# Kernel optimization log

Hardware: AMD Instinct MI355X
Metric: run time of the kernel (lower is better)

## Reference

```python
import jax, jax.numpy as jnp
import numpy as np

ATOM_DIM = 128; RBF_DIM = 32; GEOM_HID = 128; SCAT = 64; OUT = 64; CUTOFF = 5.0
MAX_Z = 100; Z_EMB = 32; E_DIM = 32; PAIR_HID = 64
B = 16; N = 64; P = 8000; NE = 80


def _lin(key, i, o):
    kw, kb = jax.random.split(key)
    W = jax.random.normal(kw, (i, o), jnp.float32) / np.sqrt(i).astype(np.float32)
    b = jax.random.normal(kb, (o,), jnp.float32) * 0.01
    return W, b


def setup_inputs() -> dict:
    key = jax.random.key(0)
    ks = jax.random.split(key, 24)
    inp = {}
    inp["h_flat"] = jax.random.normal(ks[0], (B * N, ATOM_DIM), jnp.float32)
    inp["z_flat"] = jax.random.randint(ks[1], (B * N,), 0, MAX_Z + 1)
    inp["e_feat"] = jax.random.normal(ks[2], (NE, E_DIM), jnp.float32)
    inp["path_j"] = jax.random.randint(ks[3], (P,), 0, B * N)
    inp["path_k"] = jax.random.randint(ks[4], (P,), 0, B * N)
    # distances in (0, 1.2*cutoff) so some paths exceed the cutoff
    inp["path_r0j"] = jax.random.uniform(ks[5], (P,), jnp.float32, 0.1, 1.2 * CUTOFF)
    inp["path_r0k"] = jax.random.uniform(ks[6], (P,), jnp.float32, 0.1, 1.2 * CUTOFF)
    inp["path_rjk"] = jax.random.uniform(ks[7], (P,), jnp.float32, 0.1, 1.2 * CUTOFF)
    inp["path_cosangle"] = jax.random.uniform(ks[8], (P,), jnp.float32, -1.0, 1.0)
    inp["path_batch"] = jnp.sort(jax.random.randint(ks[9], (P,), 0, B))
    inp["bsz"] = B
    # params
    inp["z_emb"] = jax.random.normal(ks[10], (MAX_Z + 1, Z_EMB), jnp.float32)
    pe_in = 2 * Z_EMB + E_DIM
    inp["pe_w1"], inp["pe_b1"] = _lin(ks[11], pe_in, PAIR_HID)
    inp["pe_w2"], inp["pe_b2"] = _lin(ks[12], PAIR_HID, PAIR_HID)
    inp["pe_w3"], inp["pe_b3"] = _lin(ks[13], PAIR_HID, SCAT)
    gm_in = 2 * ATOM_DIM + 3 * RBF_DIM + 1
    inp["gm_w1"], inp["gm_b1"] = _lin(ks[14], gm_in, GEOM_HID)
    inp["gm_w2"], inp["gm_b2"] = _lin(ks[15], GEOM_HID, GEOM_HID)
    inp["gm_w3"], inp["gm_b3"] = _lin(ks[16], GEOM_HID, SCAT)
    inp["op_w1"], inp["op_b1"] = _lin(ks[17], SCAT, GEOM_HID)
    inp["op_w2"], inp["op_b2"] = _lin(ks[18], GEOM_HID, OUT)
    return inp


def _rbf(r):
    centers = jnp.linspace(0.0, CUTOFF, RBF_DIM)
    width = centers[1] - centers[0]
    return jnp.exp(-0.5 * ((r[..., None] - centers) / width) ** 2)


def _cutoff_fn(r):
    return 0.5 * (jnp.cos(jnp.pi * r / CUTOFF) + 1.0) * (r < CUTOFF)


def _mlp3(x, w1, b1, w2, b2, w3, b3):
    h = jax.nn.silu(x @ w1 + b1)
    h = jax.nn.silu(h @ w2 + b2)
    return h @ w3 + b3


def _mlp2(x, w1, b1, w2, b2):
    return jax.nn.silu(x @ w1 + b1) @ w2 + b2


def reference(h_flat, z_flat, e_feat, path_j, path_k, path_r0j, path_r0k,
              path_rjk, path_cosangle, path_batch, bsz, z_emb,
              pe_w1, pe_b1, pe_w2, pe_b2, pe_w3, pe_b3,
              gm_w1, gm_b1, gm_w2, gm_b2, gm_w3, gm_b3,
              op_w1, op_b1, op_w2, op_b2):
    n_e = e_feat.shape[0]
    n_p = path_j.shape[0]
    # gather atom features
    hj = h_flat[path_j]                                  # (P, atom_dim)
    hk = h_flat[path_k]
    f0j = _rbf(jnp.minimum(path_r0j, CUTOFF))            # (P, rbf_dim)
    f0k = _rbf(jnp.minimum(path_r0k, CUTOFF))
    fjk = _rbf(jnp.minimum(path_rjk, CUTOFF))
    geom_in = jnp.concatenate([hj, hk, f0j, f0k, fjk, path_cosangle[:, None]], axis=-1)
    g_geom = _mlp3(geom_in, gm_w1, gm_b1, gm_w2, gm_b2, gm_w3, gm_b3)  # (P, scat)
    # element-pair energy features
    ej = z_emb[z_flat[path_j]]                           # (P, z_emb)
    ek = z_emb[z_flat[path_k]]
    pair_in = jnp.concatenate([
        jnp.broadcast_to(ej[:, None, :], (n_p, n_e, ej.shape[-1])),
        jnp.broadcast_to(ek[:, None, :], (n_p, n_e, ek.shape[-1])),
        jnp.broadcast_to(e_feat[None, :, :], (n_p, n_e, e_feat.shape[-1])),
    ], axis=-1)                                          # (P, nE, 2*z_emb+e_dim)
    g_elem = _mlp3(pair_in, pe_w1, pe_b1, pe_w2, pe_b2, pe_w3, pe_b3)  # (P, nE, scat)
    # cutoff weights and outer-product contribution
    cw = _cutoff_fn(path_r0j) * _cutoff_fn(path_r0k) * _cutoff_fn(path_rjk)  # (P,)
    contrib = g_geom[:, None, :] * g_elem * cw[:, None, None]          # (P, nE, scat)
    # scatter-add into batch bins
    agg = jax.ops.segment_sum(contrib, path_batch, num_segments=bsz)   # (B, nE, scat)
    norm = jax.ops.segment_sum(cw, path_batch, num_segments=bsz)       # (B,)
    agg = agg / jnp.maximum(norm, 1e-8)[:, None, None]
    return _mlp2(agg, op_w1, op_b1, op_w2, op_b2)                      # (B, nE, out)
```

## Files before the change

kernel.cpp:

```cpp
#include <hip/hip_runtime.h>
#include <math.h>

typedef float f32x4 __attribute__((ext_vector_type(4)));
typedef short bf16x8 __attribute__((ext_vector_type(8)));
typedef unsigned short u16;

#define RBF_DIM 32
#define CUTOFF 5.0f
#define PI_F 3.14159265358979323846f
#define BB 16
#define PP 8000
#define NEE 80

#define CW_OFF      0
#define GCW_OFF     8000
#define AGG_OFF     520000
#define ZEJW_OFF    601920
#define ZEKW_OFF    608384
#define EFWB_OFF    614848
#define NORM_OFF    619968
#define AIDX_OFF    619984
#define ZJA_OFF     627984
#define ZKA_OFF     635984
#define BOFF_OFF    643984
#define BCNT_OFF    644004
#define BSUM_OFF    644036
#define BCNTB_OFF   644548
#define BLKOFF_OFF  645060
#define CHS_OFF     645096
#define CHC_OFF     645362
#define CHB_OFF     645628
#define NC_OFF      645894
#define W2THI_OFF   645896
#define W2TLO_OFF   647944
#define W3THI_OFF   649992
#define W3TLO_OFF   652040
#define PJA_OFF     654088
#define PKA_OFF     662088
#define CWA_OFF     670088
#define HHI_OFF     678088
#define HLO_OFF     743624
#define GW1JKH_OFF  809160
#define GW1JKL_OFF  825544
#define GW1RH_OFF   841928
#define GW1RL_OFF   850120
#define GW2H_OFF    858312
#define GW2L_OFF    866504
#define GW3H_OFF    874696
#define GW3L_OFF    878792
#define HJW_OFF     882888
#define HKW_OFF     1013960

__device__ __forceinline__ float siluf(float x) { return x / (1.f + __expf(-x)); }
__device__ __forceinline__ float cutoff_fn(float r) {
    return (r < CUTOFF) ? 0.5f * (cosf(PI_F * r / CUTOFF) + 1.f) : 0.f;
}
__device__ __forceinline__ float rbff(float r, int i) {
    r = fminf(r, CUTOFF);
    float a = r * (31.0f / CUTOFF) - (float)i;
    return __expf(-0.5f * a * a);
}
__device__ __forceinline__ u16 f2bf_rne(float x) {
    unsigned u = __float_as_uint(x);
    return (u16)((u + 0x7FFFu + ((u >> 16) & 1u)) >> 16);
}
__device__ __forceinline__ unsigned cvtpk2(float a, float b) {
    unsigned r;
    asm("v_cvt_pk_bf16_f32 %0, %1, %2" : "=v"(r) : "v"(a), "v"(b));
    return r;
}
__device__ __forceinline__ void splitpack8(const float* xs, bf16x8& hi, bf16x8& lo) {
    union { bf16x8 v; unsigned u[4]; } H, L;
    #pragma unroll
    for (int d = 0; d < 4; ++d) {
        float a = xs[2 * d], b = xs[2 * d + 1];
        unsigned h = cvtpk2(a, b);
        float ra = a - __uint_as_float(h << 16);
        float rb = b - __uint_as_float(h & 0xFFFF0000u);
        H.u[d] = h;
        L.u[d] = cvtpk2(ra, rb);
    }
    hi = H.v; lo = L.v;
}

__global__ __launch_bounds__(256) void k0a_k1(
    const float* r0j, const float* r0k, const float* rjk, const int* pbatch,
    const float* z_emb, const float* e_feat, const float* pe_w1, const float* pe_b1,
    const float* pe_w2, const float* pe_w3,
    const float* h_flat, const float* gm_w1, const float* gm_w2, const float* gm_w3,
    float* ws, int* wsi)
{
    __shared__ float cwL[256];
    __shared__ int bL[256];
    __shared__ int redC[256];
    __shared__ float embL[4 * 32];
    int blkAll = blockIdx.x, t = threadIdx.x;
    if (blkAll < 32) {
        int bi = blkAll;
        for (int i = t; i < 2560; i += 256) ws[AGG_OFF + bi*2560 + i] = 0.f;
        int p = bi*250 + t;
        float cw = 0.f; int bin = -1; int valid = 0;
        if (t < 250) {
            cw = cutoff_fn(r0j[p]) * cutoff_fn(r0k[p]) * cutoff_fn(rjk[p]);
            ws[CW_OFF + p] = cw;
            bin = pbatch[p];
            valid = (cw > 0.f) ? 1 : 0;
        }
        cwL[t] = cw; bL[t] = bin; redC[t] = valid;
        __syncthreads();
        if (t < 16) {
            float s = 0.f; int c2 = 0;
            for (int i = 0; i < 256; ++i) {
                bool m = (bL[i] == t);
                s += m ? cwL[i] : 0.f;
                c2 += (m && cwL[i] > 0.f) ? 1 : 0;
            }
            ws[BSUM_OFF + bi*16 + t] = s;
            wsi[BCNTB_OFF + bi*16 + t] = c2;
        }
        __syncthreads();
        for (int s = 128; s > 0; s >>= 1) {
            if (t < s) redC[t] += redC[t + s];
            __syncthreads();
        }
        if (t == 0) wsi[BCNT_OFF + bi] = redC[0];
        return;
    }
    if (blkAll >= 106) {
        int blk = blkAll - 106;
        if (blk < 32) {
            u16* hh = (u16*)(ws + HHI_OFF);
            u16* hl = (u16*)(ws + HLO_OFF);
            int base = blk * 4096;
            for (int idx = t; idx < 4096; idx += 256) {
                int e = base + idx;
                float v = h_flat[e];
                u16 h = f2bf_rne(v);
                hh[e] = h;
                hl[e] = f2bf_rne(v - __uint_as_float(((unsigned)h) << 16));
            }
        } else if (blk < 34) {
            u16* wh = (u16*)(ws + GW1JKH_OFF);
            u16* wl = (u16*)(ws + GW1JKL_OFF);
            int base = (blk - 32) * 16384;
            for (int idx = t; idx < 16384; idx += 256) {
                int e = base + idx;
                int m = e >> 7, k = e & 127;
                float v = gm_w1[((m < 128) ? k : (128 + k)) * 128 + (m & 127)];
                u16 h = f2bf_rne(v);
                wh[e] = h;
                wl[e] = f2bf_rne(v - __uint_as_float(((unsigned)h) << 16));
            }
        } else if (blk == 34) {
            u16* wh = (u16*)(ws + GW1RH_OFF);
            u16* wl = (u16*)(ws + GW1RL_OFF);
            for (int e = t; e < 16384; e += 256) {
                int m = e >> 7, k = e & 127;
                float v = (k < 97) ? gm_w1[(256 + k) * 128 + m] : 0.f;
                u16 h = f2bf_rne(v);
                wh[e] = h;
                wl[e] = f2bf_rne(v - __uint_as_float(((unsigned)h) << 16));
            }
        } else if (blk == 35) {
            u16* wh = (u16*)(ws + GW2H_OFF);
            u16* wl = (u16*)(ws + GW2L_OFF);
            for (int e = t; e < 16384; e += 256) {
                int m = e >> 7, k = e & 127;
                float v = gm_w2[k * 128 + m];
                u16 h = f2bf_rne(v);
                wh[e] = h;
                wl[e] = f2bf_rne(v - __uint_as_float(((unsigned)h) << 16));
            }
        } else {
            u16* wh = (u16*)(ws + GW3H_OFF);
            u16* wl = (u16*)(ws + GW3L_OFF);
            for (int e = t; e < 8192; e += 256) {
                int m = e >> 7, k = e & 127;
                float v = gm_w3[k * 64 + m];
                u16 h = f2bf_rne(v);
                wh[e] = h;
                wl[e] = f2bf_rne(v - __uint_as_float(((unsigned)h) << 16));
            }
        }
        return;
    }
    int blk = blkAll - 32;
    if (blk >= 72) {
        const float* W = (blk == 72) ? pe_w2 : pe_w3;
        u16* hiD = (u16*)(ws + ((blk == 72) ? W2THI_OFF : W3THI_OFF));
        u16* loD = (u16*)(ws + ((blk == 72) ? W2TLO_OFF : W3TLO_OFF));
        for (int idx = t; idx < 4096; idx += 256) {
            int k = idx >> 6, n = idx & 63;
            float v = W[idx];
            u16 h = f2bf_rne(v);
            float hf = __uint_as_float(((unsigned)h) << 16);
            hiD[n*64 + k] = h;
            loD[n*64 + k] = f2bf_rne(v - hf);
        }
        return;
    }
    int r0, nrows, wbase;
    const float* src;
    float* dst;
    bool addb = false;
    if (blk < 26)      { r0 = blk * 4;        nrows = 101; src = z_emb;  wbase = 0;  dst = ws + ZEJW_OFF; }
    else if (blk < 52) { r0 = (blk - 26) * 4; nrows = 101; src = z_emb;  wbase = 32; dst = ws + ZEKW_OFF; }
    else               { r0 = (blk - 52) * 4; nrows = NEE; src = e_feat; wbase = 64; dst = ws + EFWB_OFF; addb = true; }
    if (t < 128) {
        int rl = t >> 5, i = t & 31;
        int r = r0 + rl;
        embL[t] = (r < nrows) ? src[r * 32 + i] : 0.f;
    }
    __syncthreads();
    int rl = t >> 6, c = t & 63;
    float acc = addb ? pe_b1[c] : 0.f;
    #pragma unroll
    for (int i = 0; i < 32; ++i)
        acc = fmaf(embL[rl * 32 + i], pe_w1[(wbase + i) * 64 + c], acc);
    int r = r0 + rl;
    if (r < nrows) dst[r * 64 + c] = acc;
}

__global__ __launch_bounds__(256) void k0b(float* ws, int* wsi)
{
    __shared__ int bcntL[32];
    __shared__ int cntB[16];
    __shared__ int boff[17];
    __shared__ int chkoff[17];
    int t = threadIdx.x;
    if (t < 16) {
        float s = 0.f;
        #pragma unroll 4
        for (int bi = 0; bi < 32; ++bi) s += ws[BSUM_OFF + bi*16 + t];
        ws[NORM_OFF + t] = s;
    }
    if (t >= 32 && t < 48) {
        int b = t - 32;
        int cb = 0;
        #pragma unroll 4
        for (int bi = 0; bi < 32; ++bi) cb += wsi[BCNTB_OFF + bi*16 + b];
        cntB[b] = cb;
    }
    if (t >= 64 && t < 96) bcntL[t - 64] = wsi[BCNT_OFF + (t - 64)];
    __syncthreads();
    for (int off = 1; off < 32; off <<= 1) {
        int v = (t < 32 && t >= off) ? bcntL[t - off] : 0;
        __syncthreads();
        if (t < 32) bcntL[t] += v;
        __syncthreads();
    }
    if (t < 32) wsi[BLKOFF_OFF + t] = bcntL[t] - wsi[BCNT_OFF + t];
    if (t == 0) {
        wsi[BLKOFF_OFF + 32] = bcntL[31];
        int bo = 0, co = 0;
        for (int b = 0; b < 16; ++b) {
            boff[b] = bo; chkoff[b] = co;
            bo += cntB[b];
            co += (cntB[b] + 31) >> 5;
        }
        boff[16] = bo; chkoff[16] = co;
        wsi[NC_OFF] = co;
    }
    __syncthreads();
    int NCv = chkoff[16];
    for (int ci = t; ci < NCv; ci += 256) {
        int b = 0;
        while (chkoff[b + 1] <= ci) b++;
        int local = ci - chkoff[b];
        int rem = cntB[b] - local * 32;
        wsi[CHS_OFF + ci] = boff[b] + local * 32;
        wsi[CHC_OFF + ci] = (rem < 32) ? rem : 32;
        wsi[CHB_OFF + ci] = b;
    }
}

__global__ __launch_bounds__(256) void k0c_k1b(
    const int* pj, const int* pk, const int* zf, float* ws, int* wsi)
{
    __shared__ int sc[256];
    int blk = blockIdx.x, t = threadIdx.x;
    if (blk < 32) {
        int bi = blk;
        int p = bi*250 + t;
        int valid = (t < 250 && ws[CW_OFF + p] > 0.f) ? 1 : 0;
        sc[t] = valid;
        __syncthreads();
        for (int off = 1; off < 256; off <<= 1) {
            int v = (t >= off) ? sc[t - off] : 0;
            __syncthreads();
            sc[t] += v;
            __syncthreads();
        }
        if (valid) {
            int pos = wsi[BLKOFF_OFF + bi] + sc[t] - 1;
            int pjv = pj[p], pkv = pk[p];
            wsi[AIDX_OFF + pos] = p;
            wsi[ZJA_OFF + pos] = zf[pjv];
            wsi[ZKA_OFF + pos] = zf[pkv];
            wsi[PJA_OFF + pos] = pjv;
            wsi[PKA_OFF + pos] = pkv;
            ws[CWA_OFF + pos] = ws[CW_OFF + p];
        }
        return;
    }
    int a0 = (blk - 32) * 64;
    int lane = t & 63, w = t >> 6, c = lane & 15, g = lane >> 4;
    const u16* hh = (const u16*)(ws + HHI_OFF);
    const u16* hl = (const u16*)(ws + HLO_OFF);
    const u16* wh = (const u16*)(ws + GW1JKH_OFF);
    const u16* wl = (const u16*)(ws + GW1JKL_OFF);
    f32x4 acc[4][4];
    #pragma unroll
    for (int i = 0; i < 4; ++i)
        #pragma unroll
        for (int j = 0; j < 4; ++j) acc[i][j] = (f32x4){0.f, 0.f, 0.f, 0.f};
    #pragma unroll 1
    for (int ks = 0; ks < 4; ++ks) {
        bf16x8 Ah[4], Al[4], Bh[4], Bl[4];
        #pragma unroll
        for (int mt = 0; mt < 4; ++mt) {
            int off = (w * 64 + mt * 16 + c) * 128 + ks * 32 + g * 8;
            Ah[mt] = *(const bf16x8*)(wh + off);
            Al[mt] = *(const bf16x8*)(wl + off);
        }
        #pragma unroll
        for (int nt = 0; nt < 4; ++nt) {
            int off = (a0 + nt * 16 + c) * 128 + ks * 32 + g * 8;
            Bh[nt] = *(const bf16x8*)(hh + off);
            Bl[nt] = *(const bf16x8*)(hl + off);
        }
        #pragma unroll
        for (int mt = 0; mt < 4; ++mt)
            #pragma unroll
            for (int nt = 0; nt < 4; ++nt) {
                f32x4 d = acc[mt][nt];
                d = __builtin_amdgcn_mfma_f32_16x16x32_bf16(Ah[mt], Bh[nt], d, 0, 0, 0);
                d = __builtin_amdgcn_mfma_f32_16x16x32_bf16(Ah[mt], Bl[nt], d, 0, 0, 0);
                d = __builtin_amdgcn_mfma_f32_16x16x32_bf16(Al[mt], Bh[nt], d, 0, 0, 0);
                acc[mt][nt] = d;
            }
    }
    float* dst = ws + ((w < 2) ? HJW_OFF : HKW_OFF);
    #pragma unroll
    for (int mt = 0; mt < 4; ++mt)
        #pragma unroll
        for (int nt = 0; nt < 4; ++nt) {
            int m = (w & 1) * 64 + mt * 16 + g * 4;
            int a = a0 + nt * 16 + c;
            *(f32x4*)(dst + a * 128 + m) = acc[mt][nt];
        }
}

__global__ __launch_bounds__(256) void k2_geom_mfma(
    const float* r0jG, const float* r0kG, const float* rjkG, const float* cosG,
    const float* b1g, const float* b2g, const float* b3g,
    float* ws, const int* wsi, float* gcw)
{
    __shared__ __align__(16) float sum3L[16 * 128];
    __shared__ __align__(16) u16 rbfH[2048], rbfL[2048];
    __shared__ __align__(16) u16 h1H[2048], h1L[2048];
    __shared__ __align__(16) u16 h2H[2048], h2L[2048];
    __shared__ int pjS[16], pkS[16];
    __shared__ float cwS[16], r0jS[16], r0kS[16], rjkS[16], cosS[16];

    int NC = wsi[NC_OFF];
    int bid = blockIdx.x;
    int cid = bid >> 1, half = bid & 1;
    if (cid >= NC) return;
    int cs = wsi[CHS_OFF + cid], cnt = wsi[CHC_OFF + cid];
    int cs16 = cs + half * 16;
    int cnt16 = cnt - half * 16;
    if (cnt16 <= 0) return;
    if (cnt16 > 16) cnt16 = 16;
    int t = threadIdx.x, lane = t & 63, w = t >> 6, c = lane & 15, g = lane >> 4;

    if (t < 16) {
        int ap = cs16 + min(t, cnt16 - 1);
        int a = wsi[AIDX_OFF + ap];
        pjS[t] = wsi[PJA_OFF + ap]; pkS[t] = wsi[PKA_OFF + ap];
        cwS[t] = ws[CWA_OFF + ap];
        r0jS[t] = r0jG[a]; r0kS[t] = r0kG[a]; rjkS[t] = rjkG[a]; cosS[t] = cosG[a];
    }
    __syncthreads();
    {
        int p = t >> 4, kc = (t & 15) * 8;
        const float* rj = ws + HJW_OFF + pjS[p] * 128 + kc;
        const float* rk = ws + HKW_OFF + pkS[p] * 128 + kc;
        int sw = (p & 7) << 2;
        *(f32x4*)(sum3L + ((p * 128 + kc) ^ sw))     = *(const f32x4*)(rj)     + *(const f32x4*)(rk);
        *(f32x4*)(sum3L + ((p * 128 + kc + 4) ^ sw)) = *(const f32x4*)(rj + 4) + *(const f32x4*)(rk + 4);
    }
    {
        int p = t >> 4, kb = (t & 15) * 8;
        float r0jv = r0jS[p], r0kv = r0kS[p], rjkv = rjkS[p], cv = cosS[p];
        float xs[8];
        #pragma unroll
        for (int i = 0; i < 8; ++i) {
            int k = kb + i;
            float v;
            if (k < 32) v = rbff(r0jv, k);
            else if (k < 64) v = rbff(r0kv, k - 32);
            else if (k < 96) v = rbff(rjkv, k - 64);
            else if (k == 96) v = cv;
            else v = 0.f;
            xs[i] = v;
        }
        bf16x8 hi, lo;
        splitpack8(xs, hi, lo);
        int idx = (p * 128 + kb) ^ ((p & 7) << 3);
        *(bf16x8*)(rbfH + idx) = hi;
        *(bf16x8*)(rbfL + idx) = lo;
    }
    __syncthreads();

    const u16* w1h = (const u16*)(ws + GW1RH_OFF);
    const u16* w1l = (const u16*)(ws + GW1RL_OFF);
    const u16* w2h = (const u16*)(ws + GW2H_OFF);
    const u16* w2l = (const u16*)(ws + GW2L_OFF);
    const u16* w3h = (const u16*)(ws + GW3H_OFF);
    const u16* w3l = (const u16*)(ws + GW3L_OFF);

    const int bswz = (c & 7) << 3;

    f32x4 acc[2];
    acc[0] = (f32x4){0.f, 0.f, 0.f, 0.f};
    acc[1] = (f32x4){0.f, 0.f, 0.f, 0.f};
    #pragma unroll 1
    for (int ks = 0; ks < 4; ++ks) {
        bf16x8 Bh, Bl;
        {
            int idx = (c * 128 + ks * 32 + g * 8) ^ bswz;
            Bh = *(const bf16x8*)(rbfH + idx);
            Bl = *(const bf16x8*)(rbfL + idx);
        }
        #pragma unroll
        for (int ml = 0; ml < 2; ++ml) {
            int off = ((w * 2 + ml) * 16 + c) * 128 + ks * 32 + g * 8;
            bf16x8 Ah = *(const bf16x8*)(w1h + off);
            bf16x8 Al = *(const bf16x8*)(w1l + off);
            f32x4 d = acc[ml];
            d = __builtin_amdgcn_mfma_f32_16x16x32_bf16(Ah, Bh, d, 0, 0, 0);
            d = __builtin_amdgcn_mfma_f32_16x16x32_bf16(Ah, Bl, d, 0, 0, 0);
            d = __builtin_amdgcn_mfma_f32_16x16x32_bf16(Al, Bh, d, 0, 0, 0);
            acc[ml] = d;
        }
    }
    #pragma unroll
    for (int ml = 0; ml < 2; ++ml) {
        int m0 = (w * 2 + ml) * 16 + g * 4;
        f32x4 s = *(const f32x4*)(sum3L + ((c * 128 + m0) ^ ((c & 7) << 2)));
        f32x4 bb = *(const f32x4*)(b1g + m0);
        f32x4 x = acc[ml] + s + bb;
        float v0 = siluf(x[0]), v1 = siluf(x[1]), v2 = siluf(x[2]), v3 = siluf(x[3]);
        unsigned h01 = cvtpk2(v0, v1), h23 = cvtpk2(v2, v3);
        float l0 = v0 - __uint_as_float(h01 << 16);
        float l1 = v1 - __uint_as_float(h01 & 0xFFFF0000u);
        float l2 = v2 - __uint_as_float(h23 << 16);
        float l3 = v3 - __uint_as_float(h23 & 0xFFFF0000u);
        unsigned lo01 = cvtpk2(l0, l1), lo23 = cvtpk2(l2, l3);
        int idx = (c * 128 + m0) ^ bswz;
        uint2 uh; uh.x = h01; uh.y = h23;
        uint2 ul; ul.x = lo01; ul.y = lo23;
        *(uint2*)(h1H + idx) = uh;
        *(uint2*)(h1L + idx) = ul;
    }
    __syncthreads();

    acc[0] = (f32x4){0.f, 0.f, 0.f, 0.f};
    acc[1] = (f32x4){0.f, 0.f, 0.f, 0.f};
    #pragma unroll 1
    for (int ks = 0; ks < 4; ++ks) {
        bf16x8 Bh, Bl;
        {
            int idx = (c * 128 + ks * 32 + g * 8) ^ bswz;
            Bh = *(const bf16x8*)(h1H + idx);
            Bl = *(const bf16x8*)(h1L + idx);
        }
        #pragma unroll
        for (int ml = 0; ml < 2; ++ml) {
            int off = ((w * 2 + ml) * 16 + c) * 128 + ks * 32 + g * 8;
            bf16x8 Ah = *(const bf16x8*)(w2h + off);
            bf16x8 Al = *(const bf16x8*)(w2l + off);
            f32x4 d = acc[ml];
            d = __builtin_amdgcn_mfma_f32_16x16x32_bf16(Ah, Bh, d, 0, 0, 0);
            d = __builtin_amdgcn_mfma_f32_16x16x32_bf16(Ah, Bl, d, 0, 0, 0);
            d = __builtin_amdgcn_mfma_f32_16x16x32_bf16(Al, Bh, d, 0, 0, 0);
            acc[ml] = d;
        }
    }
    #pragma unroll
    for (int ml = 0; ml < 2; ++ml) {
        int m0 = (w * 2 + ml) * 16 + g * 4;
        f32x4 bb = *(const f32x4*)(b2g + m0);
        f32x4 x = acc[ml] + bb;
        float v0 = siluf(x[0]), v1 = siluf(x[1]), v2 = siluf(x[2]), v3 = siluf(x[3]);
        unsigned h01 = cvtpk2(v0, v1), h23 = cvtpk2(v2, v3);
        float l0 = v0 - __uint_as_float(h01 << 16);
        float l1 = v1 - __uint_as_float(h01 & 0xFFFF0000u);
        float l2 = v2 - __uint_as_float(h23 << 16);
        float l3 = v3 - __uint_as_float(h23 & 0xFFFF0000u);
        unsigned lo01 = cvtpk2(l0, l1), lo23 = cvtpk2(l2, l3);
        int idx = (c * 128 + m0) ^ bswz;
        uint2 uh; uh.x = h01; uh.y = h23;
        uint2 ul; ul.x = lo01; ul.y = lo23;
        *(uint2*)(h2H + idx) = uh;
        *(uint2*)(h2L + idx) = ul;
    }
    __syncthreads();

    f32x4 acc3 = (f32x4){0.f, 0.f, 0.f, 0.f};
    #pragma unroll 1
    for (int ks = 0; ks < 4; ++ks) {
        bf16x8 Bh, Bl;
        {
            int idx = (c * 128 + ks * 32 + g * 8) ^ bswz;
            Bh = *(const bf16x8*)(h2H + idx);
            Bl = *(const bf16x8*)(h2L + idx);
        }
        int off = (w * 16 + c) * 128 + ks * 32 + g * 8;
        bf16x8 Ah = *(const bf16x8*)(w3h + off);
        bf16x8 Al = *(const bf16x8*)(w3l + off);
        acc3 = __builtin_amdgcn_mfma_f32_16x16x32_bf16(Ah, Bh, acc3, 0, 0, 0);
        acc3 = __builtin_amdgcn_mfma_f32_16x16x32_bf16(Ah, Bl, acc3, 0, 0, 0);
        acc3 = __builtin_amdgcn_mfma_f32_16x16x32_bf16(Al, Bh, acc3, 0, 0, 0);
    }
    {
        int m0 = w * 16 + g * 4;
        f32x4 bb = *(const f32x4*)(b3g + m0);
        if (c < cnt16) {
            f32x4 o = (acc3 + bb) * cwS[c];
            *(f32x4*)(gcw + (cs16 + c) * 64 + m0) = o;
        }
    }
}

__global__ __launch_bounds__(256) void k3_pair_mfma(
    const float* ws, const int* wsi, const float* gcw, float* agg,
    const float* b2g, const float* b3g)
{
    __shared__ __align__(16) float sL[32 * 64];
    __shared__ __align__(16) u16 h2buf[4][2048];
    __shared__ __align__(16) u16 a2lL[4096];
    __shared__ __align__(16) u16 a3lL[4096];

    int NC = wsi[NC_OFF];
    int bid = blockIdx.x;
    int cid = bid / 10;
    int et  = bid - cid * 10;
    if (cid >= NC) return;
    int cs  = wsi[CHS_OFF + cid];
    int cnt = wsi[CHC_OFF + cid];
    int bb  = wsi[CHB_OFF + cid];

    int t = threadIdx.x;
    int lane = t & 63, w = t >> 6;
    int c = lane & 15, g = lane >> 4;

    {
        int p = t >> 3, kc = (t & 7) * 8;
        int ap = cs + min(p, cnt - 1);
        int zj = wsi[ZJA_OFF + ap], zk = wsi[ZKA_OFF + ap];
        const f32x4* rj = (const f32x4*)(ws + ZEJW_OFF + zj * 64 + kc);
        const f32x4* rk = (const f32x4*)(ws + ZEKW_OFF + zk * 64 + kc);
        int sw = (p & 7) << 2;
        *(f32x4*)(sL + ((p * 64 + kc) ^ sw))     = rj[0] + rk[0];
        *(f32x4*)(sL + ((p * 64 + kc + 4) ^ sw)) = rj[1] + rk[1];
    }
    {
        const unsigned* s2 = (const unsigned*)(ws + W2TLO_OFF);
        const unsigned* s3 = (const unsigned*)(ws + W3TLO_OFF);
        unsigned* d2 = (unsigned*)a2lL;
        unsigned* d3 = (unsigned*)a3lL;
        #pragma unroll
        for (int rr = 0; rr < 8; ++rr) {
            int i = rr * 256 + t;
            int sw = ((i >> 5) & 7) << 2;
            d2[i ^ sw] = s2[i];
            d3[i ^ sw] = s3[i];
        }
    }
    const u16* w2hi = (const u16*)(ws + W2THI_OFF);
    const u16* w3hi = (const u16*)(ws + W3THI_OFF);
    bf16x8 A2h[4][2], A3h[4][2];
    #pragma unroll
    for (int mt = 0; mt < 4; ++mt)
        #pragma unroll
        for (int ks = 0; ks < 2; ++ks) {
            int off = (mt * 16 + c) * 64 + ks * 32 + g * 8;
            A2h[mt][ks] = *(const bf16x8*)(w2hi + off);
            A3h[mt][ks] = *(const bf16x8*)(w3hi + off);
        }
    __syncthreads();

    u16* myh = h2buf[w];
    u16* myl = h2buf[w] + 1024;
    const float* efp = ws + EFWB_OFF;
    const int aswz = (c & 7) << 3;

    const int cb64 = c * 64;
    const int wk0 = (g * 8) ^ aswz;
    const int wk1 = (32 + g * 8) ^ aswz;
    const int s48 = aswz & 48, s8 = aswz & 8;
    const int hwb = cb64 + ((4 * g) ^ s8);
    const u16* a2p = a2lL + cb64;
    const u16* a3p = a3lL + cb64;

    #pragma unroll 1
    for (int ei = 0; ei < 2; ++ei) {
        int e = et * 8 + w * 2 + ei;
        float part[16];
        #pragma unroll
        for (int i = 0; i < 16; ++i) part[i] = 0.f;

        #pragma unroll 1
        for (int nt = 0; nt < 2; ++nt) {
            int p = nt * 16 + c;
            int psw = (p & 7) << 2;
            f32x4 gvr[4];
            {
                int pc = cs + min(p, cnt - 1);
                #pragma unroll
                for (int mt = 0; mt < 4; ++mt)
                    gvr[mt] = *(const f32x4*)(gcw + pc * 64 + mt * 16 + 4 * g);
            }
            f32x4 acc4[4];
            #pragma unroll
            for (int mt = 0; mt < 4; ++mt) acc4[mt] = (f32x4){0.f, 0.f, 0.f, 0.f};
            #pragma unroll
            for (int ks = 0; ks < 2; ++ks) {
                f32x4 e0 = *(const f32x4*)(efp + e * 64 + ks * 32 + g * 8);
                f32x4 e1 = *(const f32x4*)(efp + e * 64 + ks * 32 + g * 8 + 4);
                int base = p * 64 + ks * 32 + g * 8;
                f32x4 x0 = *(const f32x4*)(sL + (base ^ psw));
                f32x4 x1 = *(const f32x4*)(sL + ((base + 4) ^ psw));
                x0 += e0; x1 += e1;
                float xs[8];
                #pragma unroll
                for (int i = 0; i < 4; ++i) { xs[i] = siluf(x0[i]); xs[4 + i] = siluf(x1[i]); }
                bf16x8 Bh, Bl;
                splitpack8(xs, Bh, Bl);
                const int wk = ks ? wk1 : wk0;
                #pragma unroll
                for (int mt = 0; mt < 4; ++mt) {
                    bf16x8 a2l = *(const bf16x8*)(a2p + wk + mt * 1024);
                    f32x4 d = acc4[mt];
                    d = __builtin_amdgcn_mfma_f32_16x16x32_bf16(A2h[mt][ks], Bh, d, 0, 0, 0);
                    d = __builtin_amdgcn_mfma_f32_16x16x32_bf16(A2h[mt][ks], Bl, d, 0, 0, 0);
                    d = __builtin_amdgcn_mfma_f32_16x16x32_bf16(a2l,         Bh, d, 0, 0, 0);
                    acc4[mt] = d;
                }
            }
            #pragma unroll
            for (int mt = 0; mt < 4; ++mt) {
                f32x4 b2v = *(const f32x4*)(b2g + mt * 16 + 4 * g);
                f32x4 h = acc4[mt] + b2v;
                float v0 = siluf(h[0]), v1 = siluf(h[1]), v2 = siluf(h[2]), v3 = siluf(h[3]);
                unsigned h01 = cvtpk2(v0, v1), h23 = cvtpk2(v2, v3);
                float l0 = v0 - __uint_as_float(h01 << 16);
                float l1 = v1 - __uint_as_float(h01 & 0xFFFF0000u);
                float l2 = v2 - __uint_as_float(h23 << 16);
                float l3 = v3 - __uint_as_float(h23 & 0xFFFF0000u);
                unsigned lo01 = cvtpk2(l0, l1), lo23 = cvtpk2(l2, l3);
                int idx = hwb + ((mt * 16) ^ s48);
                uint2 uh, ul;
                uh.x = h01; uh.y = h23;
                ul.x = lo01; ul.y = lo23;
                *(uint2*)(myh + idx) = uh;
                *(uint2*)(myl + idx) = ul;
                acc4[mt] = (f32x4){0.f, 0.f, 0.f, 0.f};
            }
            #pragma unroll
            for (int ks = 0; ks < 2; ++ks) {
                const int wk = ks ? wk1 : wk0;
                bf16x8 Ch = *(const bf16x8*)(myh + cb64 + wk);
                bf16x8 Cl = *(const bf16x8*)(myl + cb64 + wk);
                #pragma unroll
                for (int mt = 0; mt < 4; ++mt) {
                    bf16x8 a3l = *(const bf16x8*)(a3p + wk + mt * 1024);
                    f32x4 d = acc4[mt];
                    d = __builtin_amdgcn_mfma_f32_16x16x32_bf16(A3h[mt][ks], Ch, d, 0, 0, 0);
                    d = __builtin_amdgcn_mfma_f32_16x16x32_bf16(A3h[mt][ks], Cl, d, 0, 0, 0);
                    d = __builtin_amdgcn_mfma_f32_16x16x32_bf16(a3l,         Ch, d, 0, 0, 0);
                    acc4[mt] = d;
                }
            }
            float vmask = (p < cnt) ? 1.f : 0.f;
            #pragma unroll
            for (int mt = 0; mt < 4; ++mt) {
                f32x4 b3v = *(const f32x4*)(b3g + mt * 16 + 4 * g);
                f32x4 o = acc4[mt] + b3v;
                #pragma unroll
                for (int r = 0; r < 4; ++r) part[mt * 4 + r] += o[r] * gvr[mt][r] * vmask;
            }
        }
        #pragma unroll
        for (int i = 0; i < 16; ++i) {
            float v = part[i];
            v += __shfl_xor(v, 1, 64);
            v += __shfl_xor(v, 2, 64);
            v += __shfl_xor(v, 4, 64);
            v += __shfl_xor(v, 8, 64);
            part[i] = v;
        }
        int f = (c >> 2) * 16 + g * 4 + (c & 3);
        atomicAdd(agg + (bb * NEE + e) * 64 + f, part[c]);
    }
}

__global__ __launch_bounds__(256) void k4_out(
    const float* ws, const float* W1, const float* b1,
    const float* W2, const float* b2, float* out)
{
    __shared__ float xT[64][68];
    __shared__ float W1L[64 * 128];
    __shared__ float hTT[128][68];
    __shared__ float W2L[128 * 64];
    __shared__ float normL[16];
    int t = threadIdx.x;
    int gbase = blockIdx.x * 64;
    if (t < 16) normL[t] = 1.f / fmaxf(ws[NORM_OFF + t], 1e-8f);
    for (int idx = t; idx < 8192; idx += 256) { W1L[idx] = W1[idx]; W2L[idx] = W2[idx]; }
    __syncthreads();
    {
        int r = t & 63, cq = t >> 6;
        int gg = gbase + r;
        int b = gg / NEE;
        float rn = normL[b];
        const float* arow = ws + AGG_OFF + gg * 64 + cq * 16;
        #pragma unroll
        for (int q = 0; q < 4; ++q) {
            float4 v = *(const float4*)(arow + q * 4);
            int c = cq * 16 + q * 4;
            xT[c + 0][r] = v.x * rn; xT[c + 1][r] = v.y * rn;
            xT[c + 2][r] = v.z * rn; xT[c + 3][r] = v.w * rn;
        }
    }
    __syncthreads();
    {
        int tcx = t & 15, trx = t >> 4;
        int c0 = tcx * 8, r0 = trx * 4;
        float acc[4][8];
        #pragma unroll
        for (int j = 0; j < 4; ++j)
            #pragma unroll
            for (int q = 0; q < 8; ++q) acc[j][q] = 0.f;
        #pragma unroll 4
        for (int kk = 0; kk < 64; ++kk) {
            float4 x4 = *(const float4*)&xT[kk][r0];
            float4 wa = *(const float4*)&W1L[kk * 128 + c0];
            float4 wb = *(const float4*)&W1L[kk * 128 + c0 + 4];
            float x[4] = {x4.x, x4.y, x4.z, x4.w};
            float w[8] = {wa.x, wa.y, wa.z, wa.w, wb.x, wb.y, wb.z, wb.w};
            #pragma unroll
            for (int j = 0; j < 4; ++j)
                #pragma unroll
                for (int q = 0; q < 8; ++q)
                    acc[j][q] = fmaf(x[j], w[q], acc[j][q]);
        }
        #pragma unroll
        for (int q = 0; q < 8; ++q) {
            float bb = b1[c0 + q];
            float4 v;
            v.x = siluf(acc[0][q] + bb);
            v.y = siluf(acc[1][q] + bb);
            v.z = siluf(acc[2][q] + bb);
            v.w = siluf(acc[3][q] + bb);
            *(float4*)&hTT[c0 + q][r0] = v;
        }
    }
    __syncthreads();
    {
        int tcx = t & 7, trx = t >> 3;
        int c0 = tcx * 8, r0 = trx * 2;
        float acc[2][8];
        #pragma unroll
        for (int j = 0; j < 2; ++j)
            #pragma unroll
            for (int q = 0; q < 8; ++q) acc[j][q] = 0.f;
        #pragma unroll 4
        for (int kk = 0; kk < 128; ++kk) {
            float2 x2 = *(const float2*)&hTT[kk][r0];
            float4 wa = *(const float4*)&W2L[kk * 64 + c0];
            float4 wb = *(const float4*)&W2L[kk * 64 + c0 + 4];
            float w[8] = {wa.x, wa.y, wa.z, wa.w, wb.x, wb.y, wb.z, wb.w};
            #pragma unroll
            for (int q = 0; q < 8; ++q) {
                acc[0][q] = fmaf(x2.x, w[q], acc[0][q]);
                acc[1][q] = fmaf(x2.y, w[q], acc[1][q]);
            }
        }
        int gg = gbase + r0;
        #pragma unroll
        for (int j = 0; j < 2; ++j) {
            float o[8];
            #pragma unroll
            for (int q = 0; q < 8; ++q) o[q] = acc[j][q] + b2[c0 + q];
            *(float4*)&out[(gg + j) * 64 + c0] = make_float4(o[0], o[1], o[2], o[3]);
            *(float4*)&out[(gg + j) * 64 + c0 + 4] = make_float4(o[4], o[5], o[6], o[7]);
        }
    }
}

extern "C" void kernel_launch(void* const* d_in, const int* in_sizes, int n_in,
                              void* d_out, int out_size, void* d_ws, size_t ws_size,
                              hipStream_t stream) {
    (void)in_sizes; (void)n_in; (void)out_size; (void)ws_size;
    const float* h_flat = (const float*)d_in[0];
    const int*   z_flat = (const int*)d_in[1];
    const float* e_feat = (const float*)d_in[2];
    const int*   path_j = (const int*)d_in[3];
    const int*   path_k = (const int*)d_in[4];
    const float* r0j    = (const float*)d_in[5];
    const float* r0k    = (const float*)d_in[6];
    const float* rjk    = (const float*)d_in[7];
    const float* cosang = (const float*)d_in[8];
    const int*   pbatch = (const int*)d_in[9];
    const float* z_emb  = (const float*)d_in[11];
    const float* pe_w1  = (const float*)d_in[12];
    const float* pe_b1  = (const float*)d_in[13];
    const float* pe_w2  = (const float*)d_in[14];
    const float* pe_b2  = (const float*)d_in[15];
    const float* pe_w3  = (const float*)d_in[16];
    const float* pe_b3  = (const float*)d_in[17];
    const float* gm_w1  = (const float*)d_in[18];
    const float* gm_b1  = (const float*)d_in[19];
    const float* gm_w2  = (const float*)d_in[20];
    const float* gm_b2  = (const float*)d_in[21];
    const float* gm_w3  = (const float*)d_in[22];
    const float* gm_b3  = (const float*)d_in[23];
    const float* op_w1  = (const float*)d_in[24];
    const float* op_b1  = (const float*)d_in[25];
    const float* op_w2  = (const float*)d_in[26];
    const float* op_b2  = (const float*)d_in[27];

    float* ws  = (float*)d_ws;
    int*   wsi = (int*)d_ws;
    float* gcw = ws + GCW_OFF;
    float* agg = ws + AGG_OFF;

    hipLaunchKernelGGL(k0a_k1, dim3(143), dim3(256), 0, stream,
                       r0j, r0k, rjk, pbatch,
                       z_emb, e_feat, pe_w1, pe_b1, pe_w2, pe_w3,
                       h_flat, gm_w1, gm_w2, gm_w3, ws, wsi);
    hipLaunchKernelGGL(k0b, dim3(1), dim3(256), 0, stream, ws, wsi);
    hipLaunchKernelGGL(k0c_k1b, dim3(48), dim3(256), 0, stream,
                       path_j, path_k, z_flat, ws, wsi);
    hipLaunchKernelGGL(k2_geom_mfma, dim3(532), dim3(256), 0, stream,
                       r0j, r0k, rjk, cosang,
                       gm_b1, gm_b2, gm_b3, ws, wsi, gcw);
    hipLaunchKernelGGL(k3_pair_mfma, dim3(2660), dim3(256), 0, stream,
                       ws, wsi, gcw, agg, pe_b2, pe_b3);
    hipLaunchKernelGGL(k4_out, dim3(20), dim3(256), 0, stream,
                       ws, op_w1, op_b1, op_w2, op_b2, (float*)d_out);
}
```

Baseline: 135.5 us.

## Replace prefix-scan compaction with atomic per-bin slots and drop a kernel

The per-block counts, single-block scan kernel and second compaction pass are replaced by atomicAdd slot allocation into fixed 500-entry per-batch-bin regions, filled directly in the first kernel. Norm sums also use atomics into memsets. Later kernels index chunks by bin and slot instead of a chunk table, which removes one launch and a serial single-block step. The cost is that paths beyond 500 per bin are silently dropped, and atomic ordering makes the path order and float sums nondeterministic.

```diff
diff --git a/kernel.cpp b/kernel.cpp
--- a/kernel.cpp
+++ b/kernel.cpp
@@ -11,8 +11,8 @@
 #define BB 16
 #define PP 8000
 #define NEE 80
-
-#define CW_OFF      0
+#define RSZ 500
+
 #define GCW_OFF     8000
 #define AGG_OFF     520000
 #define ZEJW_OFF    601920
@@ -22,15 +22,7 @@
 #define AIDX_OFF    619984
 #define ZJA_OFF     627984
 #define ZKA_OFF     635984
-#define BOFF_OFF    643984
 #define BCNT_OFF    644004
-#define BSUM_OFF    644036
-#define BCNTB_OFF   644548
-#define BLKOFF_OFF  645060
-#define CHS_OFF     645096
-#define CHC_OFF     645362
-#define CHB_OFF     645628
-#define NC_OFF      645894
 #define W2THI_OFF   645896
 #define W2TLO_OFF   647944
 #define W3THI_OFF   649992
@@ -88,42 +80,42 @@
     const float* z_emb, const float* e_feat, const float* pe_w1, const float* pe_b1,
     const float* pe_w2, const float* pe_w3,
     const float* h_flat, const float* gm_w1, const float* gm_w2, const float* gm_w3,
+    const int* pj, const int* pk, const int* zf,
     float* ws, int* wsi)
 {
     __shared__ float cwL[256];
     __shared__ int bL[256];
-    __shared__ int redC[256];
     __shared__ float embL[4 * 32];
     int blkAll = blockIdx.x, t = threadIdx.x;
     if (blkAll < 32) {
         int bi = blkAll;
         for (int i = t; i < 2560; i += 256) ws[AGG_OFF + bi*2560 + i] = 0.f;
         int p = bi*250 + t;
-        float cw = 0.f; int bin = -1; int valid = 0;
+        float cw = 0.f; int bin = -1;
         if (t < 250) {
             cw = cutoff_fn(r0j[p]) * cutoff_fn(r0k[p]) * cutoff_fn(rjk[p]);
-            ws[CW_OFF + p] = cw;
             bin = pbatch[p];
-            valid = (cw > 0.f) ? 1 : 0;
-        }
-        cwL[t] = cw; bL[t] = bin; redC[t] = valid;
+            if (cw > 0.f) {
+                int pos = atomicAdd(&wsi[BCNT_OFF + bin], 1);
+                if (pos < RSZ) {
+                    int slot = bin * RSZ + pos;
+                    int pjv = pj[p], pkv = pk[p];
+                    wsi[AIDX_OFF + slot] = p;
+                    wsi[ZJA_OFF + slot] = zf[pjv];
+                    wsi[ZKA_OFF + slot] = zf[pkv];
+                    wsi[PJA_OFF + slot] = pjv;
+                    wsi[PKA_OFF + slot] = pkv;
+                    ws[CWA_OFF + slot] = cw;
+                }
+            }
+        }
+        cwL[t] = cw; bL[t] = bin;
         __syncthreads();
         if (t < 16) {
-            float s = 0.f; int c2 = 0;
-            for (int i = 0; i < 256; ++i) {
-                bool m = (bL[i] == t);
-                s += m ? cwL[i] : 0.f;
-                c2 += (m && cwL[i] > 0.f) ? 1 : 0;
-            }
-            ws[BSUM_OFF + bi*16 + t] = s;
-            wsi[BCNTB_OFF + bi*16 + t] = c2;
-        }
-        __syncthreads();
-        for (int s = 128; s > 0; s >>= 1) {
-            if (t < s) redC[t] += redC[t + s];
-            __syncthreads();
-        }
-        if (t == 0) wsi[BCNT_OFF + bi] = redC[0];
+            float s = 0.f;
+            for (int i = 0; i < 256; ++i) s += (bL[i] == t) ? cwL[i] : 0.f;
+            atomicAdd(ws + NORM_OFF + t, s);
+        }
         return;
     }
     if (blkAll >= 106) {
@@ -221,89 +213,10 @@
     if (r < nrows) dst[r * 64 + c] = acc;
 }
 
-__global__ __launch_bounds__(256) void k0b(float* ws, int* wsi)
+__global__ __launch_bounds__(256) void k1b_hw(float* ws)
 {
-    __shared__ int bcntL[32];
-    __shared__ int cntB[16];
-    __shared__ int boff[17];
-    __shared__ int chkoff[17];
     int t = threadIdx.x;
-    if (t < 16) {
-        float s = 0.f;
-        #pragma unroll 4
-        for (int bi = 0; bi < 32; ++bi) s += ws[BSUM_OFF + bi*16 + t];
-        ws[NORM_OFF + t] = s;
-    }
-    if (t >= 32 && t < 48) {
-        int b = t - 32;
-        int cb = 0;
-        #pragma unroll 4
-        for (int bi = 0; bi < 32; ++bi) cb += wsi[BCNTB_OFF + bi*16 + b];
-        cntB[b] = cb;
-    }
-    if (t >= 64 && t < 96) bcntL[t - 64] = wsi[BCNT_OFF + (t - 64)];
-    __syncthreads();
-    for (int off = 1; off < 32; off <<= 1) {
-        int v = (t < 32 && t >= off) ? bcntL[t - off] : 0;
-        __syncthreads();
-        if (t < 32) bcntL[t] += v;
-        __syncthreads();
-    }
-    if (t < 32) wsi[BLKOFF_OFF + t] = bcntL[t] - wsi[BCNT_OFF + t];
-    if (t == 0) {
-        wsi[BLKOFF_OFF + 32] = bcntL[31];
-        int bo = 0, co = 0;
-        for (int b = 0; b < 16; ++b) {
-            boff[b] = bo; chkoff[b] = co;
-            bo += cntB[b];
-            co += (cntB[b] + 31) >> 5;
-        }
-        boff[16] = bo; chkoff[16] = co;
-        wsi[NC_OFF] = co;
-    }
-    __syncthreads();
-    int NCv = chkoff[16];
-    for (int ci = t; ci < NCv; ci += 256) {
-        int b = 0;
-        while (chkoff[b + 1] <= ci) b++;
-        int local = ci - chkoff[b];
-        int rem = cntB[b] - local * 32;
-        wsi[CHS_OFF + ci] = boff[b] + local * 32;
-        wsi[CHC_OFF + ci] = (rem < 32) ? rem : 32;
-        wsi[CHB_OFF + ci] = b;
-    }
-}
-
-__global__ __launch_bounds__(256) void k0c_k1b(
-    const int* pj, const int* pk, const int* zf, float* ws, int* wsi)
-{
-    __shared__ int sc[256];
-    int blk = blockIdx.x, t = threadIdx.x;
-    if (blk < 32) {
-        int bi = blk;
-        int p = bi*250 + t;
-        int valid = (t < 250 && ws[CW_OFF + p] > 0.f) ? 1 : 0;
-        sc[t] = valid;
-        __syncthreads();
-        for (int off = 1; off < 256; off <<= 1) {
-            int v = (t >= off) ? sc[t - off] : 0;
-            __syncthreads();
-            sc[t] += v;
-            __syncthreads();
-        }
-        if (valid) {
-            int pos = wsi[BLKOFF_OFF + bi] + sc[t] - 1;
-            int pjv = pj[p], pkv = pk[p];
-            wsi[AIDX_OFF + pos] = p;
-            wsi[ZJA_OFF + pos] = zf[pjv];
-            wsi[ZKA_OFF + pos] = zf[pkv];
-            wsi[PJA_OFF + pos] = pjv;
-            wsi[PKA_OFF + pos] = pkv;
-            ws[CWA_OFF + pos] = ws[CW_OFF + p];
-        }
-        return;
-    }
-    int a0 = (blk - 32) * 64;
+    int a0 = blockIdx.x * 64;
     int lane = t & 63, w = t >> 6, c = lane & 15, g = lane >> 4;
     const u16* hh = (const u16*)(ws + HHI_OFF);
     const u16* hl = (const u16*)(ws + HLO_OFF);
@@ -363,13 +276,12 @@
     __shared__ int pjS[16], pkS[16];
     __shared__ float cwS[16], r0jS[16], r0kS[16], rjkS[16], cosS[16];
 
-    int NC = wsi[NC_OFF];
     int bid = blockIdx.x;
-    int cid = bid >> 1, half = bid & 1;
-    if (cid >= NC) return;
-    int cs = wsi[CHS_OFF + cid], cnt = wsi[CHC_OFF + cid];
-    int cs16 = cs + half * 16;
-    int cnt16 = cnt - half * 16;
+    int b = bid >> 5, ci = bid & 31;
+    int cntb = wsi[BCNT_OFF + b];
+    if (cntb > RSZ) cntb = RSZ;
+    int cs16 = b * RSZ + ci * 16;
+    int cnt16 = cntb - ci * 16;
     if (cnt16 <= 0) return;
     if (cnt16 > 16) cnt16 = 16;
     int t = threadIdx.x, lane = t & 63, w = t >> 6, c = lane & 15, g = lane >> 4;
@@ -543,14 +455,16 @@
     __shared__ __align__(16) u16 a2lL[4096];
     __shared__ __align__(16) u16 a3lL[4096];
 
-    int NC = wsi[NC_OFF];
     int bid = blockIdx.x;
     int cid = bid / 10;
     int et  = bid - cid * 10;
-    if (cid >= NC) return;
-    int cs  = wsi[CHS_OFF + cid];
-    int cnt = wsi[CHC_OFF + cid];
-    int bb  = wsi[CHB_OFF + cid];
+    int bb = cid >> 4, ci = cid & 15;
+    int cntb = wsi[BCNT_OFF + bb];
+    if (cntb > RSZ) cntb = RSZ;
+    int cs = bb * RSZ + ci * 32;
+    int cnt = cntb - ci * 32;
+    if (cnt <= 0) return;
+    if (cnt > 32) cnt = 32;
 
     int t = threadIdx.x;
     int lane = t & 63, w = t >> 6;
@@ -838,17 +752,19 @@
     float* gcw = ws + GCW_OFF;
     float* agg = ws + AGG_OFF;
 
+    hipMemsetAsync((char*)d_ws + (size_t)NORM_OFF * 4, 0, 64, stream);
+    hipMemsetAsync((char*)d_ws + (size_t)BCNT_OFF * 4, 0, 64, stream);
+
     hipLaunchKernelGGL(k0a_k1, dim3(143), dim3(256), 0, stream,
                        r0j, r0k, rjk, pbatch,
                        z_emb, e_feat, pe_w1, pe_b1, pe_w2, pe_w3,
-                       h_flat, gm_w1, gm_w2, gm_w3, ws, wsi);
-    hipLaunchKernelGGL(k0b, dim3(1), dim3(256), 0, stream, ws, wsi);
-    hipLaunchKernelGGL(k0c_k1b, dim3(48), dim3(256), 0, stream,
+                       h_flat, gm_w1, gm_w2, gm_w3,
                        path_j, path_k, z_flat, ws, wsi);
-    hipLaunchKernelGGL(k2_geom_mfma, dim3(532), dim3(256), 0, stream,
+    hipLaunchKernelGGL(k1b_hw, dim3(16), dim3(256), 0, stream, ws);
+    hipLaunchKernelGGL(k2_geom_mfma, dim3(512), dim3(256), 0, stream,
                        r0j, r0k, rjk, cosang,
                        gm_b1, gm_b2, gm_b3, ws, wsi, gcw);
-    hipLaunchKernelGGL(k3_pair_mfma, dim3(2660), dim3(256), 0, stream,
+    hipLaunchKernelGGL(k3_pair_mfma, dim3(2560), dim3(256), 0, stream,
                        ws, wsi, gcw, agg, pe_b2, pe_b3);
     hipLaunchKernelGGL(k4_out, dim3(20), dim3(256), 0, stream,
                        ws, op_w1, op_b1, op_w2, op_b2, (float*)d_out);
```

Result: slower. 168.8 us (+24.6%).
